# Kernel optimization log

Hardware: AMD Instinct MI355X
Metric: run time of the kernel (lower is better)

Reference implementation:

```python
import jax, jax.numpy as jnp
import numpy as np
import math

B, IN, OUT = 32, 8192, 8192
DENSITY = 0.15

def _inverse_softplus(v):
    return math.log(math.expm1(v))

def setup_inputs() -> dict:
    key = jax.random.key(0)
    k1, k2, k3, k4 = jax.random.split(key, 4)
    inputs = jax.random.normal(k1, (B, IN), dtype=jnp.float32)
    active = jax.random.uniform(k2, (OUT, IN)) < DENSITY
    sign = jnp.where(jax.random.uniform(k3, (OUT, IN)) < 0.5, 1, -1)
    weight_state = jnp.where(active, sign, 0).astype(jnp.int32)
    # log_scale initialized so softplus(log_scale) = 1/sqrt(in_features)
    log_scale = jnp.full((OUT,), _inverse_softplus(1.0 / math.sqrt(IN)), dtype=jnp.float32)
    bias = jax.random.normal(k4, (OUT,), dtype=jnp.float32) * 0.01
    return {"inputs": inputs, "log_scale": log_scale, "bias": bias, "weight_state": weight_state}

def reference(inputs, log_scale, bias, weight_state):
    # scale = softplus(log_scale).clamp_min(1e-4), per output channel
    scale = jnp.maximum(jax.nn.softplus(log_scale), 1e-4)  # [OUT]
    # effective_weight = ternary_state * scale[:, None]; out = x @ W^T + b
    w = weight_state.astype(inputs.dtype) * scale[:, None]  # [OUT, IN]
    return jnp.einsum('bi,oi->bo', inputs, w) + bias
```

## Files before the change

### kernel.cpp

```cpp
#include <hip/hip_runtime.h>
#include <hip/hip_bf16.h>
#include <cmath>


#define K_SZ   8192
#define N_SZ   8192
#define B_SZ   32
#define KSPLIT 8
#define KSPAN  (K_SZ / KSPLIT)
#define NHALF  16
#define BN     64

typedef __attribute__((ext_vector_type(8))) short bf16x8;
typedef __attribute__((ext_vector_type(4))) float f32x4;

__device__ __forceinline__ unsigned pack_rn(float lo, float hi) {
  unsigned ul = __builtin_bit_cast(unsigned, lo) + 0x8000u;
  unsigned uh = __builtin_bit_cast(unsigned, hi) + 0x8000u;
  return (ul >> 16) | (uh & 0xFFFF0000u);
}
__device__ __forceinline__ unsigned pack_w(int w0, int w1) {
  unsigned u0 = __builtin_bit_cast(unsigned, (float)w0);
  unsigned u1 = __builtin_bit_cast(unsigned, (float)w1);
  return (u0 >> 16) | (u1 & 0xFFFF0000u);
}

__device__ __forceinline__ void dma16(const int* g, int* l) {
  __builtin_amdgcn_global_load_lds(
      (const __attribute__((address_space(1))) unsigned*)g,
      (__attribute__((address_space(3))) unsigned*)l, 16, 0, 0);
}

__global__ void xprep(const float* __restrict__ X, uint4* __restrict__ Xr) {
  int t = blockIdx.x * blockDim.x + threadIdx.x;
  int lane = t & 63;
  int chunk = t >> 6;
  int kb = chunk >> 1;
  int mt = chunk & 1;
  int row = mt * 16 + (lane & 15);
  int k0 = kb * 32 + (lane >> 4) * 8;
  const float* p = X + (size_t)row * K_SZ + k0;
  float4 a = *(const float4*)p;
  float4 b = *(const float4*)(p + 4);
  uint4 o;
  o.x = pack_rn(a.x, a.y); o.y = pack_rn(a.z, a.w);
  o.z = pack_rn(b.x, b.y); o.w = pack_rn(b.z, b.w);
  Xr[t] = o;
}

__global__ __launch_bounds__(256, 3) void tmm(
    const int*   __restrict__ W,
    const uint4* __restrict__ Xr,
    float*       __restrict__ part) {
  __shared__ int lds[4][2][1024];

  const int tid  = threadIdx.x;
  const int w    = tid >> 6;
  const int lane = tid & 63;
  const int q    = lane >> 4;
  const int r    = lane & 15;
  const int nb   = blockIdx.x * BN;
  const int kh   = blockIdx.y;
  const int lh   = lane >> 4, l15 = lane & 15;

  const int* gp[4];
  #pragma unroll
  for (int j = 0; j < 4; ++j) {
    int rp = j * 4 + lh;
    int c  = l15 ^ rp;
    gp[j] = W + (size_t)(nb + w * 16 + rp) * K_SZ + (size_t)kh * KSPAN + c * 4;
  }
  #pragma unroll
  for (int j = 0; j < 4; ++j) dma16(gp[j], &lds[w][0][j * 256]);

  const int kbb = kh * (KSPAN / 32);
  uint4 am[2][4];
  #pragma unroll
  for (int s = 0; s < 2; ++s) {
    am[0][s * 2 + 0] = Xr[(size_t)((kbb + s) * 2 + 0) * 64 + lane];
    am[0][s * 2 + 1] = Xr[(size_t)((kbb + s) * 2 + 1) * 64 + lane];
  }

  f32x4 acc0 = {0.f, 0.f, 0.f, 0.f};
  f32x4 acc1 = {0.f, 0.f, 0.f, 0.f};

  #pragma unroll 2
  for (int h = 0; h < NHALF; ++h) {
    const int cb = h & 1, nbuf = cb ^ 1;
    if (h + 1 < NHALF) {
      #pragma unroll
      for (int j = 0; j < 4; ++j) dma16(gp[j] + (h + 1) * 64, &lds[w][nbuf][j * 256]);
      const int kb2 = kbb + (h + 1) * 2;
      #pragma unroll
      for (int s = 0; s < 2; ++s) {
        am[nbuf][s * 2 + 0] = Xr[(size_t)((kb2 + s) * 2 + 0) * 64 + lane];
        am[nbuf][s * 2 + 1] = Xr[(size_t)((kb2 + s) * 2 + 1) * 64 + lane];
      }
    }
    const int* buf = &lds[w][cb][0];
    #pragma unroll
    for (int s = 0; s < 2; ++s) {
      const int c0 = s * 8 + q * 2;
      int4 lo = *(const int4*)&buf[(r * 16 + ((c0)     ^ r)) * 4];
      int4 hi = *(const int4*)&buf[(r * 16 + ((c0 + 1) ^ r)) * 4];
      union { unsigned u[4]; bf16x8 v; } Bf;
      Bf.u[0] = pack_w(lo.x, lo.y); Bf.u[1] = pack_w(lo.z, lo.w);
      Bf.u[2] = pack_w(hi.x, hi.y); Bf.u[3] = pack_w(hi.z, hi.w);
      acc0 = __builtin_amdgcn_mfma_f32_16x16x32_bf16(
                 __builtin_bit_cast(bf16x8, am[cb][s * 2 + 0]), Bf.v, acc0, 0, 0, 0);
      acc1 = __builtin_amdgcn_mfma_f32_16x16x32_bf16(
                 __builtin_bit_cast(bf16x8, am[cb][s * 2 + 1]), Bf.v, acc1, 0, 0, 0);
    }
  }

  const int o = nb + w * 16 + r;
  float* pb = part + (size_t)kh * B_SZ * N_SZ + o;
  #pragma unroll
  for (int rg = 0; rg < 4; ++rg) {
    pb[(size_t)(q * 4 + rg) * N_SZ]        = acc0[rg];
    pb[(size_t)(16 + q * 4 + rg) * N_SZ]   = acc1[rg];
  }
}

__global__ void reduce_k(const float* __restrict__ part,
                         const float* __restrict__ ls,
                         const float* __restrict__ bias,
                         float* __restrict__ out) {
  int idx = blockIdx.x * 256 + threadIdx.x;
  int o = idx & (N_SZ - 1);
  float s = 0.f;
  #pragma unroll
  for (int kh = 0; kh < KSPLIT; ++kh)
    s += part[(size_t)kh * B_SZ * N_SZ + idx];
  float sp = log1pf(expf(ls[o]));
  out[idx] = s * fmaxf(sp, 1e-4f) + bias[o];
}

extern "C" void kernel_launch(void* const* d_in, const int* in_sizes, int n_in,
                              void* d_out, int out_size, void* d_ws, size_t ws_size,
                              hipStream_t stream) {
  const float* X  = (const float*)d_in[0];
  const float* ls = (const float*)d_in[1];
  const float* bs = (const float*)d_in[2];
  const int*   W  = (const int*)d_in[3];
  float* out  = (float*)d_out;
  uint4* Xr   = (uint4*)d_ws;
  float* part = (float*)((char*)d_ws + (512 << 10));

  xprep<<<128, 256, 0, stream>>>(X, Xr);
  dim3 grid(N_SZ / BN, KSPLIT);
  tmm<<<grid, 256, 0, stream>>>(W, Xr, part);
  reduce_k<<<(B_SZ * N_SZ) / 256, 256, 0, stream>>>(part, ls, bs, out);
}
```

Before: 412.2 us.

## Prefetch ternary weights in registers, convert to bf16 once before staging in LDS

Replaces the global-to-LDS DMA double buffer with register-staged weight loads. The weights are converted to bf16 before being written into a padded single-buffer LDS tile, and the next 128-wide K tile is prefetched into registers while the current one is consumed by MFMAs. The K split drops from 8 to 4, which halves the partial-sum traffic and the work in the reduction kernel but also halves the grid size. Occupancy is lowered to 2 blocks per CU in exchange for more loads in flight per thread. The aim is to hide weight-stream latency better and to avoid repeated int-to-bf16 packing from LDS.

Result: faster. 375.6 us (-8.9%).

```diff
diff --git a/kernel.cpp b/kernel.cpp
--- a/kernel.cpp
+++ b/kernel.cpp
@@ -6,10 +6,12 @@
 #define K_SZ   8192
 #define N_SZ   8192
 #define B_SZ   32
-#define KSPLIT 8
+#define KSPLIT 4
 #define KSPAN  (K_SZ / KSPLIT)
-#define NHALF  16
+#define BK     128
+#define STEPS  (KSPAN / BK)
 #define BN     64
+#define LDB    136
 
 typedef __attribute__((ext_vector_type(8))) short bf16x8;
 typedef __attribute__((ext_vector_type(4))) float f32x4;
@@ -23,12 +25,6 @@
   unsigned u0 = __builtin_bit_cast(unsigned, (float)w0);
   unsigned u1 = __builtin_bit_cast(unsigned, (float)w1);
   return (u0 >> 16) | (u1 & 0xFFFF0000u);
-}
-
-__device__ __forceinline__ void dma16(const int* g, int* l) {
-  __builtin_amdgcn_global_load_lds(
-      (const __attribute__((address_space(1))) unsigned*)g,
-      (__attribute__((address_space(3))) unsigned*)l, 16, 0, 0);
 }
 
 __global__ void xprep(const float* __restrict__ X, uint4* __restrict__ Xr) {
@@ -48,11 +44,11 @@
   Xr[t] = o;
 }
 
-__global__ __launch_bounds__(256, 3) void tmm(
+__global__ __launch_bounds__(256, 2) void tmm(
     const int*   __restrict__ W,
     const uint4* __restrict__ Xr,
     float*       __restrict__ part) {
-  __shared__ int lds[4][2][1024];
+  __shared__ unsigned short lds[4][16 * LDB];
 
   const int tid  = threadIdx.x;
   const int w    = tid >> 6;
@@ -61,55 +57,57 @@
   const int r    = lane & 15;
   const int nb   = blockIdx.x * BN;
   const int kh   = blockIdx.y;
-  const int lh   = lane >> 4, l15 = lane & 15;
 
-  const int* gp[4];
+  const int srow = lane >> 5;
+  const int skof = 4 * (lane & 31);
+  const int* gW0 = W + (size_t)(nb + w * 16 + srow) * K_SZ
+                     + (size_t)kh * KSPAN + skof;
+  unsigned short* lw = &lds[w][0];
+  const int kbb = kh * (KSPAN / 32);
+  const int rb  = r * LDB;
+
+  int4 wr[8];
   #pragma unroll
-  for (int j = 0; j < 4; ++j) {
-    int rp = j * 4 + lh;
-    int c  = l15 ^ rp;
-    gp[j] = W + (size_t)(nb + w * 16 + rp) * K_SZ + (size_t)kh * KSPAN + c * 4;
-  }
+  for (int j = 0; j < 8; ++j) wr[j] = *(const int4*)(gW0 + (size_t)j * 2 * K_SZ);
+  uint4 am[8];
   #pragma unroll
-  for (int j = 0; j < 4; ++j) dma16(gp[j], &lds[w][0][j * 256]);
-
-  const int kbb = kh * (KSPAN / 32);
-  uint4 am[2][4];
-  #pragma unroll
-  for (int s = 0; s < 2; ++s) {
-    am[0][s * 2 + 0] = Xr[(size_t)((kbb + s) * 2 + 0) * 64 + lane];
-    am[0][s * 2 + 1] = Xr[(size_t)((kbb + s) * 2 + 1) * 64 + lane];
+  for (int s = 0; s < 4; ++s) {
+    am[s * 2 + 0] = Xr[(size_t)((kbb + s) * 2 + 0) * 64 + lane];
+    am[s * 2 + 1] = Xr[(size_t)((kbb + s) * 2 + 1) * 64 + lane];
   }
 
   f32x4 acc0 = {0.f, 0.f, 0.f, 0.f};
   f32x4 acc1 = {0.f, 0.f, 0.f, 0.f};
 
-  #pragma unroll 2
-  for (int h = 0; h < NHALF; ++h) {
-    const int cb = h & 1, nbuf = cb ^ 1;
-    if (h + 1 < NHALF) {
+  #pragma unroll 1
+  for (int h = 0; h < STEPS; ++h) {
+    #pragma unroll
+    for (int j = 0; j < 8; ++j) {
+      uint2 p;
+      p.x = pack_w(wr[j].x, wr[j].y);
+      p.y = pack_w(wr[j].z, wr[j].w);
+      *(uint2*)&lw[(2 * j + srow) * LDB + skof] = p;
+    }
+    if (h + 1 < STEPS) {
+      const int* g = gW0 + (h + 1) * BK;
       #pragma unroll
-      for (int j = 0; j < 4; ++j) dma16(gp[j] + (h + 1) * 64, &lds[w][nbuf][j * 256]);
-      const int kb2 = kbb + (h + 1) * 2;
+      for (int j = 0; j < 8; ++j) wr[j] = *(const int4*)(g + (size_t)j * 2 * K_SZ);
+    }
+    #pragma unroll
+    for (int s = 0; s < 4; ++s) {
+      bf16x8 Bf = *(const bf16x8*)&lw[rb + s * 32 + q * 8];
+      acc0 = __builtin_amdgcn_mfma_f32_16x16x32_bf16(
+                 __builtin_bit_cast(bf16x8, am[s * 2 + 0]), Bf, acc0, 0, 0, 0);
+      acc1 = __builtin_amdgcn_mfma_f32_16x16x32_bf16(
+                 __builtin_bit_cast(bf16x8, am[s * 2 + 1]), Bf, acc1, 0, 0, 0);
+    }
+    if (h + 1 < STEPS) {
+      const int kb2 = kbb + (h + 1) * 4;
       #pragma unroll
-      for (int s = 0; s < 2; ++s) {
-        am[nbuf][s * 2 + 0] = Xr[(size_t)((kb2 + s) * 2 + 0) * 64 + lane];
-        am[nbuf][s * 2 + 1] = Xr[(size_t)((kb2 + s) * 2 + 1) * 64 + lane];
+      for (int s = 0; s < 4; ++s) {
+        am[s * 2 + 0] = Xr[(size_t)((kb2 + s) * 2 + 0) * 64 + lane];
+        am[s * 2 + 1] = Xr[(size_t)((kb2 + s) * 2 + 1) * 64 + lane];
       }
-    }
-    const int* buf = &lds[w][cb][0];
-    #pragma unroll
-    for (int s = 0; s < 2; ++s) {
-      const int c0 = s * 8 + q * 2;
-      int4 lo = *(const int4*)&buf[(r * 16 + ((c0)     ^ r)) * 4];
-      int4 hi = *(const int4*)&buf[(r * 16 + ((c0 + 1) ^ r)) * 4];
-      union { unsigned u[4]; bf16x8 v; } Bf;
-      Bf.u[0] = pack_w(lo.x, lo.y); Bf.u[1] = pack_w(lo.z, lo.w);
-      Bf.u[2] = pack_w(hi.x, hi.y); Bf.u[3] = pack_w(hi.z, hi.w);
-      acc0 = __builtin_amdgcn_mfma_f32_16x16x32_bf16(
-                 __builtin_bit_cast(bf16x8, am[cb][s * 2 + 0]), Bf.v, acc0, 0, 0, 0);
-      acc1 = __builtin_amdgcn_mfma_f32_16x16x32_bf16(
-                 __builtin_bit_cast(bf16x8, am[cb][s * 2 + 1]), Bf.v, acc1, 0, 0, 0);
     }
   }
 
@@ -117,8 +115,8 @@
   float* pb = part + (size_t)kh * B_SZ * N_SZ + o;
   #pragma unroll
   for (int rg = 0; rg < 4; ++rg) {
-    pb[(size_t)(q * 4 + rg) * N_SZ]        = acc0[rg];
-    pb[(size_t)(16 + q * 4 + rg) * N_SZ]   = acc1[rg];
+    pb[(size_t)(q * 4 + rg) * N_SZ]      = acc0[rg];
+    pb[(size_t)(16 + q * 4 + rg) * N_SZ] = acc1[rg];
   }
 }
 
```

## Use 512-thread blocks with a shared single-buffer LDS tile and finer K split

Applied to the files above, without the earlier changes.

Replaces the per-wave double-buffered LDS pipeline with one block-wide single buffer guarded by two __syncthreads per step. Block size doubles to 8 waves covering 128 output columns, and the K split doubles to 16 to raise the number of waves in flight. The activation fragments are now loaded inside each step instead of being prefetched a step ahead. In exchange, each wave loses its own load/compute overlap, gains barrier stalls, and the partial-sum buffer and reduction traffic double.

Result: faster. 392.6 us (-4.8%).

```diff
diff --git a/kernel.cpp b/kernel.cpp
--- a/kernel.cpp
+++ b/kernel.cpp
@@ -6,10 +6,10 @@
 #define K_SZ   8192
 #define N_SZ   8192
 #define B_SZ   32
-#define KSPLIT 8
+#define KSPLIT 16
 #define KSPAN  (K_SZ / KSPLIT)
-#define NHALF  16
-#define BN     64
+#define STEPS  (KSPAN / 64)
+#define BN     128
 
 typedef __attribute__((ext_vector_type(8))) short bf16x8;
 typedef __attribute__((ext_vector_type(4))) float f32x4;
@@ -33,10 +33,8 @@
 
 __global__ void xprep(const float* __restrict__ X, uint4* __restrict__ Xr) {
   int t = blockIdx.x * blockDim.x + threadIdx.x;
-  int lane = t & 63;
-  int chunk = t >> 6;
-  int kb = chunk >> 1;
-  int mt = chunk & 1;
+  int lane = t & 63, chunk = t >> 6;
+  int kb = chunk >> 1, mt = chunk & 1;
   int row = mt * 16 + (lane & 15);
   int k0 = kb * 32 + (lane >> 4) * 8;
   const float* p = X + (size_t)row * K_SZ + k0;
@@ -48,11 +46,11 @@
   Xr[t] = o;
 }
 
-__global__ __launch_bounds__(256, 3) void tmm(
+__global__ __launch_bounds__(512, 8) void tmm(
     const int*   __restrict__ W,
     const uint4* __restrict__ Xr,
     float*       __restrict__ part) {
-  __shared__ int lds[4][2][1024];
+  __shared__ int wlds[BN * 64];
 
   const int tid  = threadIdx.x;
   const int w    = tid >> 6;
@@ -61,64 +59,63 @@
   const int r    = lane & 15;
   const int nb   = blockIdx.x * BN;
   const int kh   = blockIdx.y;
-  const int lh   = lane >> 4, l15 = lane & 15;
 
   const int* gp[4];
+  int*       lb[4];
   #pragma unroll
   for (int j = 0; j < 4; ++j) {
-    int rp = j * 4 + lh;
-    int c  = l15 ^ rp;
-    gp[j] = W + (size_t)(nb + w * 16 + rp) * K_SZ + (size_t)kh * KSPAN + c * 4;
+    int p  = 16 * w + 4 * j + (lane >> 4);
+    int c  = (lane & 15) ^ (p & 15);
+    gp[j] = W + (size_t)(nb + p) * K_SZ + (size_t)kh * KSPAN + c * 4;
+    lb[j] = &wlds[(16 * w + 4 * j) * 64];
   }
+
   #pragma unroll
-  for (int j = 0; j < 4; ++j) dma16(gp[j], &lds[w][0][j * 256]);
-
-  const int kbb = kh * (KSPAN / 32);
-  uint4 am[2][4];
-  #pragma unroll
-  for (int s = 0; s < 2; ++s) {
-    am[0][s * 2 + 0] = Xr[(size_t)((kbb + s) * 2 + 0) * 64 + lane];
-    am[0][s * 2 + 1] = Xr[(size_t)((kbb + s) * 2 + 1) * 64 + lane];
-  }
+  for (int j = 0; j < 4; ++j) dma16(gp[j], lb[j]);
 
   f32x4 acc0 = {0.f, 0.f, 0.f, 0.f};
   f32x4 acc1 = {0.f, 0.f, 0.f, 0.f};
+  const int rowbase = (16 * w + r) * 64;
 
-  #pragma unroll 2
-  for (int h = 0; h < NHALF; ++h) {
-    const int cb = h & 1, nbuf = cb ^ 1;
-    if (h + 1 < NHALF) {
-      #pragma unroll
-      for (int j = 0; j < 4; ++j) dma16(gp[j] + (h + 1) * 64, &lds[w][nbuf][j * 256]);
-      const int kb2 = kbb + (h + 1) * 2;
-      #pragma unroll
-      for (int s = 0; s < 2; ++s) {
-        am[nbuf][s * 2 + 0] = Xr[(size_t)((kb2 + s) * 2 + 0) * 64 + lane];
-        am[nbuf][s * 2 + 1] = Xr[(size_t)((kb2 + s) * 2 + 1) * 64 + lane];
-      }
-    }
-    const int* buf = &lds[w][cb][0];
+  for (int h = 0; h < STEPS; ++h) {
+    __syncthreads();
+
+    const int kg = kh * (KSPAN / 32) + h * 2;
+    uint4 a00 = Xr[(size_t)((kg + 0) * 2 + 0) * 64 + lane];
+    uint4 a01 = Xr[(size_t)((kg + 0) * 2 + 1) * 64 + lane];
+    uint4 a10 = Xr[(size_t)((kg + 1) * 2 + 0) * 64 + lane];
+    uint4 a11 = Xr[(size_t)((kg + 1) * 2 + 1) * 64 + lane];
+
     #pragma unroll
-    for (int s = 0; s < 2; ++s) {
-      const int c0 = s * 8 + q * 2;
-      int4 lo = *(const int4*)&buf[(r * 16 + ((c0)     ^ r)) * 4];
-      int4 hi = *(const int4*)&buf[(r * 16 + ((c0 + 1) ^ r)) * 4];
+    for (int kb2 = 0; kb2 < 2; ++kb2) {
+      int s0 = (kb2 * 8 + 2 * q)     ^ r;
+      int s1 = (kb2 * 8 + 2 * q + 1) ^ r;
+      int4 lo = *(const int4*)&wlds[rowbase + s0 * 4];
+      int4 hi = *(const int4*)&wlds[rowbase + s1 * 4];
       union { unsigned u[4]; bf16x8 v; } Bf;
       Bf.u[0] = pack_w(lo.x, lo.y); Bf.u[1] = pack_w(lo.z, lo.w);
       Bf.u[2] = pack_w(hi.x, hi.y); Bf.u[3] = pack_w(hi.z, hi.w);
+      uint4 am0 = kb2 ? a10 : a00;
+      uint4 am1 = kb2 ? a11 : a01;
       acc0 = __builtin_amdgcn_mfma_f32_16x16x32_bf16(
-                 __builtin_bit_cast(bf16x8, am[cb][s * 2 + 0]), Bf.v, acc0, 0, 0, 0);
+                 __builtin_bit_cast(bf16x8, am0), Bf.v, acc0, 0, 0, 0);
       acc1 = __builtin_amdgcn_mfma_f32_16x16x32_bf16(
-                 __builtin_bit_cast(bf16x8, am[cb][s * 2 + 1]), Bf.v, acc1, 0, 0, 0);
+                 __builtin_bit_cast(bf16x8, am1), Bf.v, acc1, 0, 0, 0);
+    }
+
+    __syncthreads();
+    if (h + 1 < STEPS) {
+      #pragma unroll
+      for (int j = 0; j < 4; ++j) dma16(gp[j] + (h + 1) * 64, lb[j]);
     }
   }
 
-  const int o = nb + w * 16 + r;
+  const int o = nb + 16 * w + r;
   float* pb = part + (size_t)kh * B_SZ * N_SZ + o;
   #pragma unroll
   for (int rg = 0; rg < 4; ++rg) {
-    pb[(size_t)(q * 4 + rg) * N_SZ]        = acc0[rg];
-    pb[(size_t)(16 + q * 4 + rg) * N_SZ]   = acc1[rg];
+    pb[(size_t)(q * 4 + rg) * N_SZ]      = acc0[rg];
+    pb[(size_t)(16 + q * 4 + rg) * N_SZ] = acc1[rg];
   }
 }
 
@@ -149,6 +146,6 @@
 
   xprep<<<128, 256, 0, stream>>>(X, Xr);
   dim3 grid(N_SZ / BN, KSPLIT);
-  tmm<<<grid, 256, 0, stream>>>(W, Xr, part);
+  tmm<<<grid, 512, 0, stream>>>(W, Xr, part);
   reduce_k<<<(B_SZ * N_SZ) / 256, 256, 0, stream>>>(part, ls, bs, out);
 }
```
